# Performance work log

Measured on AMD Instinct MI355X. Metric: run time of the kernel, lower is better.

Reference implementation:

```python
import jax, jax.numpy as jnp
import numpy as np

WS = 2048            # window_size
STEP = WS // 2       # hop = window_size // 2
NC = WS // 2 + 1     # rfft coeffs
NB = 4               # n_blocks


def _hann():
    # periodic hann window (torch.hann_window default)
    return 0.5 - 0.5 * jnp.cos(2.0 * jnp.pi * jnp.arange(WS) / WS)


def _block(x, transfer, gain):
    # x: (b, 1, time); transfer: (NC,); gain: scalar
    b, ch, time = x.shape
    frames = time // STEP
    padded = jnp.pad(x, ((0, 0), (0, 0), (0, STEP)))
    idx = jnp.arange(frames)[:, None] * STEP + jnp.arange(WS)[None, :]
    windowed = padded[:, :, idx]                       # (b, ch, F, WS)
    spec = jnp.fft.rfft(windowed, axis=-1)             # (b, ch, F, NC) complex
    spec_t = jnp.moveaxis(spec, 2, 0)                  # (F, b, ch, NC)
    tc = transfer.astype(spec.dtype)

    # linear recurrence: out_i = transfer * (spec_i + out_{i-1})
    def step_fn(carry, s):
        out = (s + carry) * tc
        return out, out

    _, outs = jax.lax.scan(step_fn, jnp.zeros_like(spec_t[0]), spec_t)
    wins = jnp.fft.irfft(outs, n=WS, axis=-1) * _hann()  # (F, b, ch, WS)
    wins = jnp.moveaxis(wins, 0, 2)                      # (b, ch, F, WS)
    # overlap-add with hop = WS/2: split each frame into two halves
    first = wins[..., :STEP].reshape(b, ch, frames * STEP)
    second = wins[..., STEP:].reshape(b, ch, frames * STEP)
    samples = (jnp.pad(first, ((0, 0), (0, 0), (0, STEP)))
               + jnp.pad(second, ((0, 0), (0, 0), (STEP, 0))))
    return jnp.tanh(samples * gain)[..., :time]


def setup_inputs() -> dict:
    key = jax.random.key(0)
    k_x, k_b, k_s, k_g = jax.random.split(key, 4)
    x = jax.random.normal(k_x, (32, 1, 262144), dtype=jnp.float32)
    # init_transfer: sparse resonances * scaling * pitch^2
    resonances = (jax.random.uniform(k_b, (NB, NC)) < 0.01).astype(jnp.float32)
    scaling = jax.random.uniform(k_s, (NB, NC), minval=0.9, maxval=0.998)
    pitch = jnp.linspace(1.0, 0.0, NC) ** 2
    transfers = resonances * scaling * pitch[None, :]
    gains = jax.random.uniform(k_g, (NB,), minval=10.0, maxval=200.0)
    mixer = jnp.zeros((NB + 1,), dtype=jnp.float32)
    return {"x": x, "transfers": transfers, "gains": gains, "mixer": mixer}


def reference(x, transfers, gains, mixer):
    outputs = [x]
    inp = x
    for i in range(NB):
        inp = _block(inp, transfers[i], gains[i])
        outputs.append(inp)
    stacked = jnp.stack(outputs, axis=-1)          # (b, 1, time, NB+1)
    mixer_values = jax.nn.softmax(mixer)
    return jnp.sum(stacked * mixer_values, axis=-1)
```

## Files before the change

### kernel.cpp

```cpp
#include <hip/hip_runtime.h>
#include <math.h>
#include <stdint.h>

#define NB   4
#define NC   1025
#define WSZ  2048
#define STEP 1024
#define FRM  256
#define BAT  32
#define TT   262144
#define SEGS 4
#define KC   16
#define YPAD 68

#define RREV (1.0f / 2048.0f)

typedef float f2 __attribute__((ext_vector_type(2)));

__device__ __forceinline__ float tanh_fast(float z) {
    float e = __expf(2.0f * z);
    return 1.0f - 2.0f / (e + 1.0f);
}

__device__ __forceinline__ void cis_rev(int idx, float* c, float* s) {
    float rev = (float)(idx & 2047) * RREV;
    *c = __builtin_amdgcn_cosf(rev);
    *s = __builtin_amdgcn_sinf(rev);
}

__global__ __launch_bounds__(1024) void setup_kernel(
    const float* __restrict__ transfers, const float* __restrict__ mixer,
    int* __restrict__ counts, int* __restrict__ bins, float* __restrict__ tvals,
    float* __restrict__ wmix, float* __restrict__ hann, int kmax)
{
    int i = blockIdx.x, tid = threadIdx.x;
    __shared__ int wcnt[16], woff[16];
    if (i == 0) {
        float cc, ss; cis_rev(tid, &cc, &ss);
        hann[tid] = 0.5f - 0.5f * cc;
    }
    float tv = transfers[i * NC + tid];
    bool nz = (tv != 0.0f);
    unsigned long long mask = __ballot(nz);
    int lane = tid & 63, w = tid >> 6;
    int within = __popcll(mask & ((1ULL << lane) - 1ULL));
    if (lane == 0) wcnt[w] = __popcll(mask);
    __syncthreads();
    if (tid == 0) {
        int acc = 0;
        for (int q = 0; q < 16; ++q) { woff[q] = acc; acc += wcnt[q]; }
        float tvL = transfers[i * NC + 1024];
        if (tvL != 0.0f && acc < kmax) { bins[i * NC + acc] = 1024; tvals[i * NC + acc] = tvL; acc++; }
        counts[i] = (acc < kmax) ? acc : kmax;
        if (i == 0) {
            float m = mixer[0];
            for (int q = 1; q < 5; ++q) m = fmaxf(m, mixer[q]);
            float e[5], s = 0.f;
            for (int q = 0; q < 5; ++q) { e[q] = __expf(mixer[q] - m); s += e[q]; }
            for (int q = 0; q < 5; ++q) wmix[q] = e[q] / s;
        }
    }
    __syncthreads();
    if (nz) {
        int pos = woff[w] + within;
        if (pos < kmax) { bins[i * NC + pos] = tid; tvals[i * NC + pos] = tv; }
    }
}

__global__ __launch_bounds__(256) void table_kernel(
    const int* __restrict__ counts, const int* __restrict__ bins,
    float2* __restrict__ cisA, float2* __restrict__ cisB, int kmax)
{
    int i = blockIdx.x >> 2, c = blockIdx.x & 3;
    int K = counts[i];
    int tid = threadIdx.x;
    for (int j = c; j < K; j += 4) {
        int k = bins[i * NC + j];
        if (tid < 64) {
            float cc, ss; cis_rev(k * tid, &cc, &ss);
            cisA[((size_t)i * kmax + j) * 64 + tid] = make_float2(cc, ss);
        } else if (tid < 80) {
            int q = tid - 64;
            float cc, ss; cis_rev(k * 64 * q, &cc, &ss);
            cisB[((size_t)i * kmax + j) * 16 + q] = make_float2(cc, ss);
        }
    }
}

__device__ __forceinline__ void half_dft(
    const float xr[16], int K, const float2* __restrict__ cA,
    const float2* __restrict__ cB, float2* __restrict__ Hout, int lane, int w)
{
    for (int j = w; j < K; j += 8) {
        int j2 = j + 4;
        bool two = (j2 < K);
        float2 bA = cB[(size_t)j * 16 + 1];
        float2 bB = two ? cB[(size_t)j2 * 16 + 1] : bA;
        float2 wAl = cA[(size_t)j * 64 + lane];
        float2 wBl = two ? cA[(size_t)j2 * 64 + lane] : wAl;
        f2 Wr, Wi, nWi;
        Wr.x = bA.x; Wr.y = bB.x;
        Wi.x = -bA.y; Wi.y = -bB.y;
        nWi = -Wi;
        f2 hr = 0.f, hi = 0.f;
#pragma unroll
        for (int i = 15; i >= 0; --i) {
            f2 xx; xx.x = xr[i]; xx.y = xr[i];
            f2 tmp = nWi * hi + xx;
            f2 nr = Wr * hr + tmp;
            hi = Wi * hr + Wr * hi;
            hr = nr;
        }
        f2 wlc, wls;
        wlc.x = wAl.x; wlc.y = wBl.x;
        wls.x = wAl.y; wls.y = wBl.y;
        f2 re = hr * wlc + hi * wls;
        f2 im = hi * wlc - hr * wls;
        float reA = re.x, imA = im.x, reB = re.y, imB = im.y;
#pragma unroll
        for (int m = 32; m >= 1; m >>= 1) {
            reA += __shfl_xor(reA, m, 64);
            imA += __shfl_xor(imA, m, 64);
            reB += __shfl_xor(reB, m, 64);
            imB += __shfl_xor(imB, m, 64);
        }
        if (lane == 0) {
            Hout[j] = make_float2(reA, imA);
            if (two) Hout[j2] = make_float2(reB, imB);
        }
    }
}

__global__ __launch_bounds__(256, 8) void analysis_kernel(
    const float* __restrict__ x, const int* __restrict__ counts,
    const float2* __restrict__ cisA, const float2* __restrict__ cisB,
    float2* __restrict__ H, int iblk, int kmax)
{
    int wg = blockIdx.x;
    int b = wg >> 8, h = wg & 255;
    int tid = threadIdx.x;
    int lane = tid & 63, w = tid >> 6;
    int K = counts[iblk];
    const float* xb = x + (size_t)b * TT + (size_t)h * STEP;
    float xr[16];
#pragma unroll
    for (int i = 0; i < 16; ++i) xr[i] = xb[lane + (i << 6)];
    const float2* cA = cisA + (size_t)iblk * kmax * 64;
    const float2* cB = cisB + (size_t)iblk * kmax * 16;
    float2* Hout = H + (size_t)(b * FRM + h) * K;
    half_dft(xr, K, cA, cB, Hout, lane, w);
}

__global__ __launch_bounds__(256) void scan_kernel(
    float2* __restrict__ S, const int* __restrict__ counts,
    const int* __restrict__ bins, const float* __restrict__ tvals, int iblk)
{
    int K = counts[iblk];
    int wg = blockIdx.x;
    int b = wg & (BAT - 1), j0 = wg >> 5;
    int f = threadIdx.x;
    int lane = f & 63, w = f >> 6;
    __shared__ float2 wtot[4];
    for (int j = j0; j < K; j += 32) {
        float t = tvals[iblk * NC + j];
        int k = bins[iblk * NC + j];
        float2* Sb = S + (size_t)b * FRM * K + j;
        float2 h1 = Sb[(size_t)f * K];
        float2 h2 = (f < FRM - 1) ? Sb[(size_t)(f + 1) * K] : make_float2(0.f, 0.f);
        float sgn = (k & 1) ? -t : t;
        float ax = fmaf(sgn, h2.x, h1.x * t);
        float ay = fmaf(sgn, h2.y, h1.y * t);
        float td = t;
        float tp0, tp1, tp2, tp3, tp4, tp5;
#pragma unroll
        for (int s = 0; s < 6; ++s) {
            int d = 1 << s;
            if (s == 0) tp0 = td; else if (s == 1) tp1 = td; else if (s == 2) tp2 = td;
            else if (s == 3) tp3 = td; else if (s == 4) tp4 = td; else tp5 = td;
            float bx = __shfl_up(ax, d, 64);
            float by = __shfl_up(ay, d, 64);
            if (lane >= d) { ax = fmaf(td, bx, ax); ay = fmaf(td, by, ay); }
            td *= td;
        }
        if (lane == 63) wtot[w] = make_float2(ax, ay);
        __syncthreads();
        float px = 0.f, py = 0.f;
#pragma unroll
        for (int w2 = 0; w2 < 3; ++w2) {
            if (w2 < w) {
                float2 v = wtot[w2];
                px = fmaf(px, td, v.x);
                py = fmaf(py, td, v.y);
            }
        }
        int n = lane + 1;
        float fac = (n & 64) ? td : 1.0f;
        if (n & 1)  fac *= tp0;
        if (n & 2)  fac *= tp1;
        if (n & 4)  fac *= tp2;
        if (n & 8)  fac *= tp3;
        if (n & 16) fac *= tp4;
        if (n & 32) fac *= tp5;
        ax = fmaf(fac, px, ax);
        ay = fmaf(fac, py, ay);
        Sb[(size_t)f * K] = make_float2(ax, ay);
        __syncthreads();
    }
}

__device__ __forceinline__ void acc4(
    f2& q0, f2& q1, f2& q2, f2& q3, float4 e, float4 a0, float4 a1)
{
    f2 up; up.x = e.x; up.y = e.y;
    f2 vp; vp.x = e.z; vp.y = e.w;
    q0 = up * a0.x + q0; q0 = vp * a0.y + q0;
    q1 = up * a0.z + q1; q1 = vp * a0.w + q1;
    q2 = up * a1.x + q2; q2 = vp * a1.y + q2;
    q3 = up * a1.z + q3; q3 = vp * a1.w + q3;
}

__global__ __launch_bounds__(256, 5) void fused_synth_kernel(
    const float2* __restrict__ S, float2* __restrict__ H2,
    const float2* __restrict__ cisA, const float2* __restrict__ cisB,
    const int* __restrict__ counts, const int* __restrict__ bins,
    const float* __restrict__ gains, const float* __restrict__ wmix,
    const float* __restrict__ hann, const float* __restrict__ x,
    float* __restrict__ dout, int iblk, int do_an, int kmax)
{
    __shared__ float4 smem[1216];
    float4* rc = smem;
    float*  ystage = (float*)smem;
    float4* part = smem + 1088;

    int wg = blockIdx.x;
    int b = wg >> 6, s0 = (wg & 63) << 2;
    int tid = threadIdx.x;
    int n1 = tid << 2;
    int q = tid >> 4;
    int m = (tid & 15) << 2;

    int K = counts[iblk];
    const int* bl = bins + iblk * NC;
    const float2* Ob = S + (size_t)b * FRM * K;
    const float2* cA0 = cisA + (size_t)iblk * kmax * 64;
    const float2* cB0 = cisB + (size_t)iblk * kmax * 16;

    f2 p00 = 0.f, p01 = 0.f, p02 = 0.f, p03 = 0.f;
    f2 p10 = 0.f, p11 = 0.f, p12 = 0.f, p13 = 0.f;
    f2 p20 = 0.f, p21 = 0.f, p22 = 0.f, p23 = 0.f;
    f2 p30 = 0.f, p31 = 0.f, p32 = 0.f, p33 = 0.f;

    for (int c0 = 0; c0 < K; c0 += KC) {
        int cs = (K - c0 < KC) ? (K - c0) : KC;
        {
            int flat = tid >> 2;
            int seg = flat >> 4;
            int j = flat & 15;
            int jj = c0 + ((j < cs) ? j : (cs - 1));
            int q0 = (tid & 3) << 2;
            int k = bl[jj];
            float g = ((k == 0) || (k == 1024)) ? (1.0f / 2048.0f) : (2.0f / 2048.0f);
            float sg = (k & 1) ? -g : g;
            int fc = s0 + seg;
            float2 o1 = Ob[(size_t)fc * K + jj];
            float2 om = (fc > 0) ? Ob[(size_t)(fc - 1) * K + jj] : make_float2(0.f, 0.f);
            float c2r = om.x * sg, c2i = om.y * sg;
            f2 u; u.x = c2r;  u.y = o1.x * g - c2r;
            f2 v; v.x = -c2i; v.y = -(o1.y * g - c2i);
            const float2* bqp = cB0 + (size_t)jj * 16 + q0;
#pragma unroll
            for (int e = 0; e < 4; ++e) {
                float2 bq = bqp[e];
                f2 up = u * bq.x + v * bq.y;
                f2 vp = v * bq.x - u * bq.y;
                rc[(flat << 4) + q0 + e] = make_float4(up.x, up.y, vp.x, vp.y);
            }
        }
        __syncthreads();
        const float2* cAj = cA0 + ((size_t)c0 << 6) + m;
        const float4* rcq = rc + q;
        int jj = 0;
        for (; jj + 2 <= cs; jj += 2) {
            float4 a00 = *(const float4*)(cAj);
            float4 a01 = *(const float4*)(cAj + 2);
            float4 a10 = *(const float4*)(cAj + 64);
            float4 a11 = *(const float4*)(cAj + 66);
            cAj += 128;
            {
                float4 e0 = rcq[(0 * KC + jj) << 4];
                float4 e1 = rcq[(0 * KC + jj + 1) << 4];
                acc4(p00, p01, p02, p03, e0, a00, a01);
                acc4(p00, p01, p02, p03, e1, a10, a11);
            }
            {
                float4 e0 = rcq[(1 * KC + jj) << 4];
                float4 e1 = rcq[(1 * KC + jj + 1) << 4];
                acc4(p10, p11, p12, p13, e0, a00, a01);
                acc4(p10, p11, p12, p13, e1, a10, a11);
            }
            {
                float4 e0 = rcq[(2 * KC + jj) << 4];
                float4 e1 = rcq[(2 * KC + jj + 1) << 4];
                acc4(p20, p21, p22, p23, e0, a00, a01);
                acc4(p20, p21, p22, p23, e1, a10, a11);
            }
            {
                float4 e0 = rcq[(3 * KC + jj) << 4];
                float4 e1 = rcq[(3 * KC + jj + 1) << 4];
                acc4(p30, p31, p32, p33, e0, a00, a01);
                acc4(p30, p31, p32, p33, e1, a10, a11);
            }
        }
        if (jj < cs) {
            float4 a0 = *(const float4*)(cAj);
            float4 a1 = *(const float4*)(cAj + 2);
            float4 e0 = rcq[(0 * KC + jj) << 4];
            float4 e1 = rcq[(1 * KC + jj) << 4];
            float4 e2 = rcq[(2 * KC + jj) << 4];
            float4 e3 = rcq[(3 * KC + jj) << 4];
            acc4(p00, p01, p02, p03, e0, a0, a1);
            acc4(p10, p11, p12, p13, e1, a0, a1);
            acc4(p20, p21, p22, p23, e2, a0, a1);
            acc4(p30, p31, p32, p33, e3, a0, a1);
        }
        __syncthreads();
    }

    size_t base0 = (size_t)b * TT + ((size_t)s0 << 10) + (size_t)n1;
    const float* prevsrc = (iblk == 0) ? x : dout;
    float4 hv = *(const float4*)(hann + n1);
    float gain = gains[iblk];
    float wsel = (iblk == 0) ? wmix[0] : 1.0f;
    float wn = wmix[iblk + 1];
    int cw = n1 >> 6, off = n1 & 63;

#define SEG_EPI(s, A0, A1, A2, A3)                                              \
    {                                                                           \
        float4 pv = *(const float4*)(prevsrc + base0 + ((size_t)(s) << 10));    \
        float4 yv;                                                              \
        yv.x = tanh_fast(fmaf(hv.x, A0.y, A0.x) * gain);                        \
        yv.y = tanh_fast(fmaf(hv.y, A1.y, A1.x) * gain);                        \
        yv.z = tanh_fast(fmaf(hv.z, A2.y, A2.x) * gain);                        \
        yv.w = tanh_fast(fmaf(hv.w, A3.y, A3.x) * gain);                        \
        float4 dv;                                                              \
        dv.x = fmaf(wsel, pv.x, wn * yv.x);                                     \
        dv.y = fmaf(wsel, pv.y, wn * yv.y);                                     \
        dv.z = fmaf(wsel, pv.z, wn * yv.z);                                     \
        dv.w = fmaf(wsel, pv.w, wn * yv.w);                                     \
        *(float4*)(dout + base0 + ((size_t)(s) << 10)) = dv;                    \
        if (do_an) *(float4*)(ystage + (s) * 16 * YPAD + cw * YPAD + off) = yv; \
    }

    SEG_EPI(0, p00, p01, p02, p03)
    SEG_EPI(1, p10, p11, p12, p13)
    SEG_EPI(2, p20, p21, p22, p23)
    SEG_EPI(3, p30, p31, p32, p33)
#undef SEG_EPI

    if (do_an) {
        __syncthreads();
        int K2 = counts[iblk + 1];
        if (K2 > 0) {
            const float2* cA2 = cisA + (size_t)(iblk + 1) * kmax * 64;
            const float2* cB2 = cisB + (size_t)(iblk + 1) * kmax * 16;
            int jloc = tid & 15, c = tid >> 4;
            int lane = tid & 63, wv = tid >> 6;
            const float4* yp0 = (const float4*)(ystage + c * YPAD);
            const float4* yp1 = (const float4*)(ystage + 16 * YPAD + c * YPAD);
            const float4* yp2 = (const float4*)(ystage + 32 * YPAD + c * YPAD);
            const float4* yp3 = (const float4*)(ystage + 48 * YPAD + c * YPAD);
            for (int jb = 0; jb < K2; jb += 16) {
                int j = jb + jloc;
                int js = (j < K2) ? j : (K2 - 1);
                float2 w1 = cA2[(size_t)js * 64 + 1];
                float Wr = w1.x, Wi = -w1.y, nWi = w1.y;
                f2 hrA = 0.f, hiA = 0.f;
                f2 hrB = 0.f, hiB = 0.f;
#pragma unroll
                for (int i4 = 15; i4 >= 0; --i4) {
                    float4 ya = yp0[i4];
                    float4 yb = yp1[i4];
                    float4 yc = yp2[i4];
                    float4 yd = yp3[i4];
#define HSTEP(CC)                                                                   \
                    { f2 yy; yy.x = ya.CC; yy.y = yb.CC;                            \
                      f2 t = hiA * nWi + yy; f2 nr = hrA * Wr + t;                  \
                      hiA = hrA * Wi + hiA * Wr; hrA = nr; }                        \
                    { f2 yy; yy.x = yc.CC; yy.y = yd.CC;                            \
                      f2 t = hiB * nWi + yy; f2 nr = hrB * Wr + t;                  \
                      hiB = hrB * Wi + hiB * Wr; hrB = nr; }
                    HSTEP(w)
                    HSTEP(z)
                    HSTEP(y)
                    HSTEP(x)
#undef HSTEP
                }
                float2 bq = cB2[(size_t)js * 16 + c];
                f2 reA = hrA * bq.x + hiA * bq.y;
                f2 imA = hiA * bq.x - hrA * bq.y;
                f2 reB = hrB * bq.x + hiB * bq.y;
                f2 imB = hiB * bq.x - hrB * bq.y;
                float4 prA = make_float4(reA.x, imA.x, reA.y, imA.y);
                float4 prB = make_float4(reB.x, imB.x, reB.y, imB.y);
#pragma unroll
                for (int d = 16; d <= 32; d <<= 1) {
                    prA.x += __shfl_xor(prA.x, d, 64);
                    prA.y += __shfl_xor(prA.y, d, 64);
                    prA.z += __shfl_xor(prA.z, d, 64);
                    prA.w += __shfl_xor(prA.w, d, 64);
                    prB.x += __shfl_xor(prB.x, d, 64);
                    prB.y += __shfl_xor(prB.y, d, 64);
                    prB.z += __shfl_xor(prB.z, d, 64);
                    prB.w += __shfl_xor(prB.w, d, 64);
                }
                if (lane < 16) {
                    part[wv * 16 + lane] = prA;
                    part[64 + wv * 16 + lane] = prB;
                }
                __syncthreads();
                if (tid < 32) {
                    int sel = tid >> 4, t = tid & 15;
                    int j2 = jb + t;
                    if (j2 < K2) {
                        const float4* pp = part + sel * 64;
                        float4 a0 = pp[t];
                        float4 a1 = pp[16 + t];
                        float4 a2 = pp[32 + t];
                        float4 a3 = pp[48 + t];
                        float4 acc;
                        acc.x = (a0.x + a1.x) + (a2.x + a3.x);
                        acc.y = (a0.y + a1.y) + (a2.y + a3.y);
                        acc.z = (a0.z + a1.z) + (a2.z + a3.z);
                        acc.w = (a0.w + a1.w) + (a2.w + a3.w);
                        H2[(size_t)(b * FRM + s0 + sel * 2) * K2 + j2] = make_float2(acc.x, acc.y);
                        H2[(size_t)(b * FRM + s0 + sel * 2 + 1) * K2 + j2] = make_float2(acc.z, acc.w);
                    }
                }
                __syncthreads();
            }
        }
    }
}

extern "C" void kernel_launch(void* const* d_in, const int* in_sizes, int n_in,
                              void* d_out, int out_size, void* d_ws, size_t ws_size,
                              hipStream_t stream)
{
    const float* x         = (const float*)d_in[0];
    const float* transfers = (const float*)d_in[1];
    const float* gains     = (const float*)d_in[2];
    const float* mixer     = (const float*)d_in[3];
    float* dout = (float*)d_out;

    uint8_t* ws = (uint8_t*)d_ws;
    int*   counts = (int*)ws;
    int*   bins   = (int*)(ws + 64);
    float* tvals  = (float*)(ws + 64 + 16400);
    float* wmix   = (float*)(ws + 64 + 16400 + 16400);
    float* hann   = (float*)(ws + 36864);
    const size_t HDR = 65536;

    long long perk = 2LL * BAT * FRM * 8 + (long long)NB * 80 * 8;
    long long km = ((long long)ws_size - (long long)HDR) / perk;
    int kmax = (int)((km < 1) ? 1 : ((km > NC) ? NC : km));
    float2* S0 = (float2*)(ws + HDR);
    float2* S1 = S0 + (size_t)BAT * FRM * kmax;
    float2* cisA = S1 + (size_t)BAT * FRM * kmax;
    float2* cisB = cisA + (size_t)NB * kmax * 64;

    setup_kernel<<<NB, 1024, 0, stream>>>(transfers, mixer, counts, bins, tvals, wmix, hann, kmax);
    table_kernel<<<NB * 4, 256, 0, stream>>>(counts, bins, cisA, cisB, kmax);
    analysis_kernel<<<BAT * FRM, 256, 0, stream>>>(x, counts, cisA, cisB, S0, 0, kmax);

    float2* cur = S0;
    float2* nxt = S1;
    for (int i = 0; i < NB; ++i) {
        scan_kernel<<<BAT * 32, 256, 0, stream>>>(cur, counts, bins, tvals, i);
        fused_synth_kernel<<<BAT * (FRM / SEGS), 256, 0, stream>>>(cur, nxt, cisA, cisB, counts, bins,
                                                                   gains, wmix, hann, x, dout, i,
                                                                   (i < NB - 1) ? 1 : 0, kmax);
        float2* t = cur; cur = nxt; nxt = t;
    }
}
```

Baseline: 234.2 us.

## Make scan one wave per (batch, bin) with four frames per lane

Restructures the frame-recurrence scan so that each 64-lane wave handles all 256 frames of one (batch, bin) pair, with each lane doing a serial scan over four frames. A single wave-level shuffle scan combines the per-lane results, which removes the LDS cross-wave combine and both __syncthreads per bin. The grid shrinks to a quarter of its size because each workgroup now carries four independent waves. The risks are lower memory-level parallelism per wave and strided loads of four frames per lane.

```diff
diff --git a/kernel.cpp b/kernel.cpp
--- a/kernel.cpp
+++ b/kernel.cpp
@@ -156,55 +156,46 @@
     const int* __restrict__ bins, const float* __restrict__ tvals, int iblk)
 {
     int K = counts[iblk];
-    int wg = blockIdx.x;
-    int b = wg & (BAT - 1), j0 = wg >> 5;
-    int f = threadIdx.x;
-    int lane = f & 63, w = f >> 6;
-    __shared__ float2 wtot[4];
+    int gw = (blockIdx.x << 2) + (threadIdx.x >> 6);
+    int lane = threadIdx.x & 63;
+    int b = gw & (BAT - 1), j0 = gw >> 5;
     for (int j = j0; j < K; j += 32) {
         float t = tvals[iblk * NC + j];
         int k = bins[iblk * NC + j];
+        float sgn = (k & 1) ? -t : t;
         float2* Sb = S + (size_t)b * FRM * K + j;
-        float2 h1 = Sb[(size_t)f * K];
-        float2 h2 = (f < FRM - 1) ? Sb[(size_t)(f + 1) * K] : make_float2(0.f, 0.f);
-        float sgn = (k & 1) ? -t : t;
-        float ax = fmaf(sgn, h2.x, h1.x * t);
-        float ay = fmaf(sgn, h2.y, h1.y * t);
-        float td = t;
-        float tp0, tp1, tp2, tp3, tp4, tp5;
-#pragma unroll
-        for (int s = 0; s < 6; ++s) {
-            int d = 1 << s;
-            if (s == 0) tp0 = td; else if (s == 1) tp1 = td; else if (s == 2) tp2 = td;
-            else if (s == 3) tp3 = td; else if (s == 4) tp4 = td; else tp5 = td;
-            float bx = __shfl_up(ax, d, 64);
-            float by = __shfl_up(ay, d, 64);
-            if (lane >= d) { ax = fmaf(td, bx, ax); ay = fmaf(td, by, ay); }
-            td *= td;
-        }
-        if (lane == 63) wtot[w] = make_float2(ax, ay);
-        __syncthreads();
-        float px = 0.f, py = 0.f;
-#pragma unroll
-        for (int w2 = 0; w2 < 3; ++w2) {
-            if (w2 < w) {
-                float2 v = wtot[w2];
-                px = fmaf(px, td, v.x);
-                py = fmaf(py, td, v.y);
-            }
-        }
-        int n = lane + 1;
-        float fac = (n & 64) ? td : 1.0f;
-        if (n & 1)  fac *= tp0;
-        if (n & 2)  fac *= tp1;
-        if (n & 4)  fac *= tp2;
-        if (n & 8)  fac *= tp3;
-        if (n & 16) fac *= tp4;
-        if (n & 32) fac *= tp5;
-        ax = fmaf(fac, px, ax);
-        ay = fmaf(fac, py, ay);
-        Sb[(size_t)f * K] = make_float2(ax, ay);
-        __syncthreads();
+        int f0 = lane << 2;
+        float2 h1_0 = Sb[(size_t)(f0 + 0) * K];
+        float2 h1_1 = Sb[(size_t)(f0 + 1) * K];
+        float2 h1_2 = Sb[(size_t)(f0 + 2) * K];
+        float2 h1_3 = Sb[(size_t)(f0 + 3) * K];
+        float2 h1_4 = (f0 + 4 < FRM) ? Sb[(size_t)(f0 + 4) * K] : make_float2(0.f, 0.f);
+        float ax0 = fmaf(sgn, h1_1.x, h1_0.x * t), ay0 = fmaf(sgn, h1_1.y, h1_0.y * t);
+        float ax1 = fmaf(sgn, h1_2.x, h1_1.x * t), ay1 = fmaf(sgn, h1_2.y, h1_1.y * t);
+        float ax2 = fmaf(sgn, h1_3.x, h1_2.x * t), ay2 = fmaf(sgn, h1_3.y, h1_2.y * t);
+        float ax3 = fmaf(sgn, h1_4.x, h1_3.x * t), ay3 = fmaf(sgn, h1_4.y, h1_3.y * t);
+        float Ax0 = ax0,                  Ay0 = ay0;
+        float Ax1 = fmaf(t, Ax0, ax1),    Ay1 = fmaf(t, Ay0, ay1);
+        float Ax2 = fmaf(t, Ax1, ax2),    Ay2 = fmaf(t, Ay1, ay2);
+        float Ax3 = fmaf(t, Ax2, ax3),    Ay3 = fmaf(t, Ay2, ay3);
+        float t2 = t * t, t4 = t2 * t2;
+        float Px = Ax3, Py = Ay3;
+        float w = t4;
+#pragma unroll
+        for (int d = 1; d <= 32; d <<= 1) {
+            float ux = __shfl_up(Px, d, 64);
+            float uy = __shfl_up(Py, d, 64);
+            if (lane >= d) { Px = fmaf(w, ux, Px); Py = fmaf(w, uy, Py); }
+            w *= w;
+        }
+        float Cx = __shfl_up(Px, 1, 64);
+        float Cy = __shfl_up(Py, 1, 64);
+        if (lane == 0) { Cx = 0.f; Cy = 0.f; }
+        float t3 = t2 * t;
+        Sb[(size_t)(f0 + 0) * K] = make_float2(fmaf(t,  Cx, Ax0), fmaf(t,  Cy, Ay0));
+        Sb[(size_t)(f0 + 1) * K] = make_float2(fmaf(t2, Cx, Ax1), fmaf(t2, Cy, Ay1));
+        Sb[(size_t)(f0 + 2) * K] = make_float2(fmaf(t3, Cx, Ax2), fmaf(t3, Cy, Ay2));
+        Sb[(size_t)(f0 + 3) * K] = make_float2(fmaf(t4, Cx, Ax3), fmaf(t4, Cy, Ay3));
     }
 }
 
@@ -475,7 +466,7 @@
     float2* cur = S0;
     float2* nxt = S1;
     for (int i = 0; i < NB; ++i) {
-        scan_kernel<<<BAT * 32, 256, 0, stream>>>(cur, counts, bins, tvals, i);
+        scan_kernel<<<BAT * 8, 256, 0, stream>>>(cur, counts, bins, tvals, i);
         fused_synth_kernel<<<BAT * (FRM / SEGS), 256, 0, stream>>>(cur, nxt, cisA, cisB, counts, bins,
                                                                    gains, wmix, hann, x, dout, i,
                                                                    (i < NB - 1) ? 1 : 0, kmax);
```

New measurement: 235.9 us. No clear change (+0.7%).
